# Optimization experiments

Hardware: AMD Instinct MI355X
Metric: run time of the kernel (lower is better)

The kernel has to match this reference:

```python
import jax, jax.numpy as jnp
import numpy as np

B, SEQ, DIM = 2, 2048, 1024
HEADS, DIM_HEAD = 16, 64
INNER = HEADS * DIM_HEAD
SCALE = DIM_HEAD ** -0.5


def rotate_half(x):
    # pair consecutive dims (d r) with r=2: (x1, x2) -> (-x2, x1)
    xp = x.reshape(*x.shape[:-1], -1, 2)
    x1, x2 = xp[..., 0], xp[..., 1]
    return jnp.stack((-x2, x1), axis=-1).reshape(x.shape)


def apply_rotary_emb(freqs, t):
    # freqs: [n, rot_dim] angles; t: [b, h, n, d]
    rot_dim = freqs.shape[-1]
    t_rot, t_pass = t[..., :rot_dim], t[..., rot_dim:]
    t_rot = t_rot * jnp.cos(freqs) + rotate_half(t_rot) * jnp.sin(freqs)
    return jnp.concatenate([t_rot, t_pass], axis=-1)


def setup_inputs() -> dict:
    key = jax.random.key(0)
    ks = jax.random.split(key, 4)
    x = jax.random.normal(ks[0], (B, SEQ, DIM), dtype=jnp.float32)
    mask = jnp.ones((B, SEQ), dtype=bool)
    rotary_pos_emb = jax.random.uniform(ks[1], (SEQ, DIM_HEAD), dtype=jnp.float32)
    Wqkv = jax.random.normal(ks[2], (DIM, 3 * INNER), dtype=jnp.float32) * 0.02
    Wout = jax.random.normal(ks[3], (INNER, DIM), dtype=jnp.float32) * 0.02
    bout = jnp.zeros((DIM,), dtype=jnp.float32)
    return {"x": x, "mask": mask, "rotary_pos_emb": rotary_pos_emb,
            "Wqkv": Wqkv, "Wout": Wout, "bout": bout}


def reference(x, mask, rotary_pos_emb, Wqkv, Wout, bout):
    b, n, _ = x.shape
    qkv = x @ Wqkv                                   # [b, n, 3*inner]
    q, k, v = jnp.split(qkv, 3, axis=-1)

    def to_heads(t):
        return t.reshape(b, n, HEADS, DIM_HEAD).transpose(0, 2, 1, 3)  # [b,h,n,d]

    q, k, v = to_heads(q), to_heads(k), to_heads(v)
    freqs = rotary_pos_emb[:n, :]
    # NB: original applies rotary to q, k AND v
    q = apply_rotary_emb(freqs, q)
    k = apply_rotary_emb(freqs, k)
    v = apply_rotary_emb(freqs, v)
    q = q * SCALE

    dots = jnp.einsum('bhid,bhjd->bhij', q, k)       # [b,h,n,n]
    mask_value = -jnp.finfo(dots.dtype).max
    pad = mask[:, None, None, :]                     # [b,1,1,n] keep where True
    dots = jnp.where(pad, dots, mask_value)
    idx = jnp.arange(n)
    causal = idx[None, :] > idx[:, None]             # j >= i + (j-i+1) with i==j==n
    dots = jnp.where(causal[None, None], mask_value, dots)

    attn = jax.nn.softmax(dots, axis=-1)
    out = jnp.einsum('bhij,bhjd->bhid', attn, v)     # [b,h,n,d]
    out = out.transpose(0, 2, 1, 3).reshape(b, n, INNER)
    return out @ Wout + bout
```

## Files before the change

### kernel.cpp

```cpp
#include <hip/hip_runtime.h>
#include <hip/hip_bf16.h>
#include <stdint.h>

#define DEVI __device__ __forceinline__

typedef __bf16 bf16x8 __attribute__((ext_vector_type(8)));
typedef float f32x4 __attribute__((ext_vector_type(4)));
typedef float f32x16 __attribute__((ext_vector_type(16)));

static constexpr int SEQ = 2048;
static constexpr int DIM = 1024;
static constexpr int HEADS = 16;
static constexpr int NQKV = 3072;
static constexpr int MROWS = 4096;
static constexpr float QSCALE = 0.125f;
static constexpr float LOG2E = 1.4426950408889634f;

DEVI unsigned short f2bf(float f) {
  unsigned int u = __builtin_bit_cast(unsigned int, f);
  u += 0x7FFFu + ((u >> 16) & 1u);
  return (unsigned short)(u >> 16);
}

DEVI bf16x8 ld8(const unsigned short* p) {
  return __builtin_bit_cast(bf16x8, *(const uint4*)p);
}

DEVI f32x4 mfma16(bf16x8 a, bf16x8 b, f32x4 c) {
  return __builtin_amdgcn_mfma_f32_16x16x32_bf16(a, b, c, 0, 0, 0);
}

DEVI f32x16 mfma32(bf16x8 a, bf16x8 b, f32x16 c) {
  return __builtin_amdgcn_mfma_f32_32x32x16_bf16(a, b, c, 0, 0, 0);
}

DEVI void load_lds16(const void* g, void* l) {
  __builtin_amdgcn_global_load_lds((const __attribute__((address_space(1))) void*)g,
                                   (__attribute__((address_space(3))) void*)l,
                                   16, 0, 0);
}

DEVI int swz(int row, int kelem) {
  return row * 64 + (kelem ^ ((row & 7) << 3));
}

DEVI unsigned cvtpk(float lo, float hi) {
  unsigned r;
  asm("v_cvt_pk_bf16_f32 %0, %1, %2" : "=v"(r) : "v"(lo), "v"(hi));
  return r;
}

DEVI void pl32swap(unsigned& a, unsigned& b) {
  asm volatile("v_permlane32_swap_b32 %0, %1" : "+v"(a), "+v"(b));
}
DEVI float xhalf_max(float v) { return fmaxf(v, __shfl_xor(v, 32)); }
DEVI float xhalf_sum(float v) { return v + __shfl_xor(v, 32); }

__global__ __launch_bounds__(256) void k_rope_tables(const float* __restrict__ rope,
                                                     float* __restrict__ cosb,
                                                     float* __restrict__ sinb) {
  int i = blockIdx.x * 256 + threadIdx.x;
  float f = rope[i];
  cosb[i] = cosf(f);
  sinb[i] = sinf(f);
}

__global__ __launch_bounds__(256) void k_cast_bf16(const float* __restrict__ in,
                                                   unsigned short* __restrict__ out) {
  int i = blockIdx.x * 256 + threadIdx.x;
  float4 f = *(const float4*)(in + (size_t)i * 4);
  ushort4 v;
  v.x = f2bf(f.x); v.y = f2bf(f.y); v.z = f2bf(f.z); v.w = f2bf(f.w);
  *(ushort4*)(out + (size_t)i * 4) = v;
}

__global__ __launch_bounds__(256) void k_transpose_bf16(const float* __restrict__ in,
                                                        unsigned short* __restrict__ out,
                                                        int Kd, int Nd) {
  __shared__ unsigned short T[64][68];
  const int n0 = blockIdx.x * 64, k0 = blockIdx.y * 64;
  const int rr = threadIdx.x >> 4, cc = (threadIdx.x & 15) * 4;
#pragma unroll
  for (int p = 0; p < 4; ++p) {
    const int r = p * 16 + rr;
    float4 f = *(const float4*)(in + (size_t)(k0 + r) * Nd + n0 + cc);
    T[r][cc + 0] = f2bf(f.x);
    T[r][cc + 1] = f2bf(f.y);
    T[r][cc + 2] = f2bf(f.z);
    T[r][cc + 3] = f2bf(f.w);
  }
  __syncthreads();
#pragma unroll
  for (int p = 0; p < 4; ++p) {
    const int rn = p * 16 + rr;
    ushort4 v;
    v.x = T[cc + 0][rn];
    v.y = T[cc + 1][rn];
    v.z = T[cc + 2][rn];
    v.w = T[cc + 3][rn];
    *(ushort4*)(out + (size_t)(n0 + rn) * Kd + k0 + cc) = v;
  }
}

DEVI void gemm_mainloop(const unsigned short* __restrict__ A,
                        const unsigned short* __restrict__ B, int K,
                        int m0, int n0,
                        unsigned short* As, unsigned short* Bs,
                        f32x4 (&acc)[4][4]) {
  const int lane = threadIdx.x & 63;
  const int wid = threadIdx.x >> 6;
  const int wm = wid >> 1, wn = wid & 1;
  for (int kt = 0; kt < K; kt += 32) {
    __syncthreads();
#pragma unroll
    for (int i = 0; i < 2; ++i) {
      const int chunk = wid * 2 + i;
      const int row = chunk * 16 + (lane >> 2);
      const int kc = kt + (lane & 3) * 8;
      load_lds16(A + (size_t)(m0 + row) * K + kc, As + chunk * 512);
      load_lds16(B + (size_t)(n0 + row) * K + kc, Bs + chunk * 512);
    }
    __syncthreads();
    bf16x8 af[4], bfv[4];
#pragma unroll
    for (int mi = 0; mi < 4; ++mi)
      af[mi] = ld8(&As[(wm * 64 + mi * 16 + (lane & 15)) * 32 + 8 * (lane >> 4)]);
#pragma unroll
    for (int ni = 0; ni < 4; ++ni)
      bfv[ni] = ld8(&Bs[(wn * 64 + ni * 16 + (lane & 15)) * 32 + 8 * (lane >> 4)]);
#pragma unroll
    for (int mi = 0; mi < 4; ++mi)
#pragma unroll
      for (int ni = 0; ni < 4; ++ni)
        acc[mi][ni] = mfma16(af[mi], bfv[ni], acc[mi][ni]);
  }
}

__global__ __launch_bounds__(256) void k_gemm_qkv(
    const unsigned short* __restrict__ xb, const unsigned short* __restrict__ wt,
    const float* __restrict__ cosb, const float* __restrict__ sinb,
    unsigned short* __restrict__ qb, unsigned short* __restrict__ kb,
    unsigned short* __restrict__ vb) {
  __shared__ unsigned short As[128 * 32];
  __shared__ unsigned short Bs[128 * 32];
  const int m0 = blockIdx.x * 128, n0 = blockIdx.y * 128;
  f32x4 acc[4][4] = {};
  gemm_mainloop(xb, wt, DIM, m0, n0, As, Bs, acc);
  const int lane = threadIdx.x & 63, wid = threadIdx.x >> 6;
  const int wm = wid >> 1, wn = wid & 1;
#pragma unroll
  for (int mi = 0; mi < 4; ++mi) {
#pragma unroll
    for (int ni = 0; ni < 4; ++ni) {
      const int ng = n0 + wn * 64 + ni * 16 + (lane & 15);
      const int d = ng & 63;
      const int part = ng >> 10;
      const int h = (ng & 1023) >> 6;
#pragma unroll
      for (int r = 0; r < 4; ++r) {
        const int mg = m0 + wm * 64 + mi * 16 + 4 * (lane >> 4) + r;
        const int s = mg & (SEQ - 1), b = mg >> 11;
        float v = acc[mi][ni][r];
        float p = __shfl_xor(v, 1);
        float cv = cosb[(s << 6) + d], sv = sinb[(s << 6) + d];
        float rot = v * cv + ((d & 1) ? p : -p) * sv;
        const size_t bh = (size_t)(b * HEADS + h);
        if (part == 0) {
          qb[(bh * SEQ + s) * 64 + d] = f2bf(rot * (QSCALE * LOG2E));
        } else if (part == 1) {
          kb[(bh * SEQ + s) * 64 + d] = f2bf(rot);
        } else {
          vb[(bh * 64 + d) * SEQ + s] = f2bf(rot);
        }
      }
    }
  }
}

__global__ __launch_bounds__(256) void k_flash(
    const unsigned short* __restrict__ qb, const unsigned short* __restrict__ kb,
    const unsigned short* __restrict__ vtb, unsigned short* __restrict__ ao) {
  __shared__ __align__(16) unsigned short Ks[2][2][64 * 64];
  __shared__ __align__(16) unsigned short Vt[2][2][64 * 64];
  const int bh = blockIdx.x;
  const int j = blockIdx.y;
  const int tid = threadIdx.x, lane = tid & 63, wid = tid >> 6;
  const int wq = wid >> 1, wk = wid & 1;
  const int la31 = lane & 31, h = lane >> 5;
  const unsigned short* kbh = kb + (size_t)bh * SEQ * 64;
  const unsigned short* vbh = vtb + (size_t)bh * 64 * SEQ;
  const int b = bh >> 4, hh = bh & 15;
  const int sslot = ((lane & 7) ^ (lane >> 3)) * 8;
  float* mrg = (float*)&Ks[0][0][0];
  const int mbase = wq * 2176;

  auto stage = [&](int buf, int t) {
    const int kv0 = t * 64;
#pragma unroll
    for (int i = 0; i < 4; ++i) {
      const int chunk = wq * 4 + i;
      const int row = chunk * 8 + (lane >> 3);
      load_lds16(kbh + ((size_t)(kv0 + row) << 6) + sslot, &Ks[buf][wk][chunk * 512]);
      load_lds16(vbh + (size_t)row * SEQ + kv0 + sslot, &Vt[buf][wk][chunk * 512]);
    }
  };

#pragma unroll 1
  for (int hf = 0; hf < 2; ++hf) {
    const int qt = hf == 0 ? (31 - j) : j;
    const int q0 = qt * 64 + wq * 32;
    const int qr = q0 + la31;
    const unsigned short* qp = qb + ((size_t)bh * SEQ + qr) * 64;
    bf16x8 qf0 = ld8(qp + 0 + 8 * h);
    bf16x8 qf1 = ld8(qp + 16 + 8 * h);
    bf16x8 qf2 = ld8(qp + 32 + 8 * h);
    bf16x8 qf3 = ld8(qp + 48 + 8 * h);

    f32x16 o0 = {}, o1 = {};
    float m = -1e30f, l = 0.f;
    const int nkv = qt + 1;
    const int nst = (nkv + 1) >> 1;

    if (wk < nkv) stage(0, wk);
#pragma unroll 1
    for (int st = 0; st < nst; ++st) {
      const int cur = st & 1;
      const int t = 2 * st + wk;
      __syncthreads();
      { const int tn = 2 * (st + 1) + wk; if (tn < nkv) stage(cur ^ 1, tn); }

      if (t < nkv) {
        const int kv0 = t * 64;
        const unsigned short* Kc = &Ks[cur][wk][0];
        const unsigned short* Vc = &Vt[cur][wk][0];
        f32x16 st0 = {}, st1 = {};
        __builtin_amdgcn_s_setprio(1);
#pragma unroll
        for (int ks = 0; ks < 4; ++ks) {
          bf16x8 qk = (ks == 0) ? qf0 : (ks == 1) ? qf1 : (ks == 2) ? qf2 : qf3;
          st0 = mfma32(ld8(&Kc[swz(la31, 16 * ks + 8 * h)]), qk, st0);
          st1 = mfma32(ld8(&Kc[swz(32 + la31, 16 * ks + 8 * h)]), qk, st1);
        }
        __builtin_amdgcn_s_setprio(0);
        if (kv0 + 63 > q0) {
#pragma unroll
          for (int r = 0; r < 16; ++r) {
            const int kvo = (r & 3) + 8 * (r >> 2) + 4 * h;
            st0[r] = (kv0 + kvo > qr) ? -1e30f : st0[r];
            st1[r] = (kv0 + 32 + kvo > qr) ? -1e30f : st1[r];
          }
        }
        float a8[8];
#pragma unroll
        for (int i = 0; i < 8; ++i)
          a8[i] = fmaxf(fmaxf(st0[i], st0[i + 8]), fmaxf(st1[i], st1[i + 8]));
        float a4_0 = fmaxf(a8[0], a8[4]), a4_1 = fmaxf(a8[1], a8[5]);
        float a4_2 = fmaxf(a8[2], a8[6]), a4_3 = fmaxf(a8[3], a8[7]);
        float pmax = fmaxf(fmaxf(a4_0, a4_1), fmaxf(a4_2, a4_3));
        const bool nor = __all(pmax <= m + 8.f);
        float scl = 1.f;
        if (!nor) {
          const float rowmax = xhalf_max(pmax);
          const float mnew = fmaxf(m, rowmax);
          scl = exp2f(m - mnew);
          m = mnew;
        }
#pragma unroll
        for (int r = 0; r < 16; ++r) {
          st0[r] = exp2f(st0[r] - m);
          st1[r] = exp2f(st1[r] - m);
        }
        float s8[8];
#pragma unroll
        for (int i = 0; i < 8; ++i)
          s8[i] = (st0[i] + st0[i + 8]) + (st1[i] + st1[i + 8]);
        float s4_0 = s8[0] + s8[4], s4_1 = s8[1] + s8[5];
        float s4_2 = s8[2] + s8[6], s4_3 = s8[3] + s8[7];
        float psum = (s4_0 + s4_1) + (s4_2 + s4_3);
        const float rowsum = xhalf_sum(psum);
        if (nor) {
          l += rowsum;
        } else {
          l = l * scl + rowsum;
#pragma unroll
          for (int r = 0; r < 16; ++r) { o0[r] *= scl; o1[r] *= scl; }
        }

        unsigned w0 = cvtpk(st0[0], st0[1]),   w1 = cvtpk(st0[2], st0[3]);
        unsigned w2 = cvtpk(st0[4], st0[5]),   w3 = cvtpk(st0[6], st0[7]);
        unsigned w4 = cvtpk(st0[8], st0[9]),   w5 = cvtpk(st0[10], st0[11]);
        unsigned w6 = cvtpk(st0[12], st0[13]), w7 = cvtpk(st0[14], st0[15]);
        pl32swap(w0, w2); pl32swap(w1, w3); pl32swap(w4, w6); pl32swap(w5, w7);
        const bf16x8 pa0 = __builtin_bit_cast(bf16x8, (uint4){w0, w1, w2, w3});
        const bf16x8 pa1 = __builtin_bit_cast(bf16x8, (uint4){w4, w5, w6, w7});
        unsigned x0 = cvtpk(st1[0], st1[1]),   x1 = cvtpk(st1[2], st1[3]);
        unsigned x2 = cvtpk(st1[4], st1[5]),   x3 = cvtpk(st1[6], st1[7]);
        unsigned x4 = cvtpk(st1[8], st1[9]),   x5 = cvtpk(st1[10], st1[11]);
        unsigned x6 = cvtpk(st1[12], st1[13]), x7 = cvtpk(st1[14], st1[15]);
        pl32swap(x0, x2); pl32swap(x1, x3); pl32swap(x4, x6); pl32swap(x5, x7);
        const bf16x8 pa2 = __builtin_bit_cast(bf16x8, (uint4){x0, x1, x2, x3});
        const bf16x8 pa3 = __builtin_bit_cast(bf16x8, (uint4){x4, x5, x6, x7});

        __builtin_amdgcn_s_setprio(1);
        o0 = mfma32(ld8(&Vc[swz(la31, 0 + 8 * h)]), pa0, o0);
        o0 = mfma32(ld8(&Vc[swz(la31, 16 + 8 * h)]), pa1, o0);
        o0 = mfma32(ld8(&Vc[swz(la31, 32 + 8 * h)]), pa2, o0);
        o0 = mfma32(ld8(&Vc[swz(la31, 48 + 8 * h)]), pa3, o0);
        o1 = mfma32(ld8(&Vc[swz(32 + la31, 0 + 8 * h)]), pa0, o1);
        o1 = mfma32(ld8(&Vc[swz(32 + la31, 16 + 8 * h)]), pa1, o1);
        o1 = mfma32(ld8(&Vc[swz(32 + la31, 32 + 8 * h)]), pa2, o1);
        o1 = mfma32(ld8(&Vc[swz(32 + la31, 48 + 8 * h)]), pa3, o1);
        __builtin_amdgcn_s_setprio(0);
      }
    }

    __syncthreads();
    if (wk == 1) {
#pragma unroll
      for (int s = 0; s < 8; ++s) {
        f32x4 c;
        if (s < 4) { c[0]=o0[4*s]; c[1]=o0[4*s+1]; c[2]=o0[4*s+2]; c[3]=o0[4*s+3]; }
        else       { c[0]=o1[4*(s-4)]; c[1]=o1[4*(s-4)+1]; c[2]=o1[4*(s-4)+2]; c[3]=o1[4*(s-4)+3]; }
        *(f32x4*)&mrg[mbase + lane * 32 + 4 * (s ^ (lane & 7))] = c;
      }
      mrg[mbase + 2048 + lane] = m;
      mrg[mbase + 2112 + lane] = l;
    }
    __syncthreads();
    if (wk == 0) {
      const float m1 = mrg[mbase + 2048 + lane];
      const float l1 = mrg[mbase + 2112 + lane];
      const float mM = fmaxf(m, m1);
      const float sc0 = exp2f(m - mM), sc1 = exp2f(m1 - mM);
      const float lt = l * sc0 + l1 * sc1;
      const float rl = __builtin_amdgcn_rcpf(lt);
      unsigned short* aor = ao + ((size_t)(b * SEQ + qr)) * 1024 + hh * 64;
#pragma unroll
      for (int s = 0; s < 8; ++s) {
        f32x4 c = *(const f32x4*)&mrg[mbase + lane * 32 + 4 * (s ^ (lane & 7))];
        float v0, v1, v2, v3;
        if (s < 4) {
          v0 = (o0[4*s]   * sc0 + c[0] * sc1) * rl;
          v1 = (o0[4*s+1] * sc0 + c[1] * sc1) * rl;
          v2 = (o0[4*s+2] * sc0 + c[2] * sc1) * rl;
          v3 = (o0[4*s+3] * sc0 + c[3] * sc1) * rl;
        } else {
          v0 = (o1[4*(s-4)]   * sc0 + c[0] * sc1) * rl;
          v1 = (o1[4*(s-4)+1] * sc0 + c[1] * sc1) * rl;
          v2 = (o1[4*(s-4)+2] * sc0 + c[2] * sc1) * rl;
          v3 = (o1[4*(s-4)+3] * sc0 + c[3] * sc1) * rl;
        }
        uint2 uv;
        uv.x = cvtpk(v0, v1);
        uv.y = cvtpk(v2, v3);
        *(uint2*)(aor + (s < 4 ? 8 * s : 32 + 8 * (s - 4)) + 4 * h) = uv;
      }
    }
    __syncthreads();
  }
}

__global__ __launch_bounds__(256) void k_gemm_out(
    const unsigned short* __restrict__ ao, const unsigned short* __restrict__ wt,
    const float* __restrict__ bout, float* __restrict__ out) {
  __shared__ unsigned short As[128 * 32];
  __shared__ unsigned short Bs[128 * 32];
  const int m0 = blockIdx.x * 128, n0 = blockIdx.y * 128;
  f32x4 acc[4][4] = {};
  gemm_mainloop(ao, wt, DIM, m0, n0, As, Bs, acc);
  const int lane = threadIdx.x & 63, wid = threadIdx.x >> 6;
  const int wm = wid >> 1, wn = wid & 1;
#pragma unroll
  for (int mi = 0; mi < 4; ++mi) {
#pragma unroll
    for (int ni = 0; ni < 4; ++ni) {
      const int ng = n0 + wn * 64 + ni * 16 + (lane & 15);
      const float bn = bout[ng];
#pragma unroll
      for (int r = 0; r < 4; ++r) {
        const int mg = m0 + wm * 64 + mi * 16 + 4 * (lane >> 4) + r;
        out[(size_t)mg * DIM + ng] = acc[mi][ni][r] + bn;
      }
    }
  }
}

extern "C" void kernel_launch(void* const* d_in, const int* in_sizes, int n_in,
                              void* d_out, int out_size, void* d_ws, size_t ws_size,
                              hipStream_t stream) {
  const float* x    = (const float*)d_in[0];
  const float* rope = (const float*)d_in[2];
  const float* Wqkv = (const float*)d_in[3];
  const float* Wout = (const float*)d_in[4];
  const float* bout = (const float*)d_in[5];
  float* out = (float*)d_out;

  char* ws = (char*)d_ws;
  unsigned short* xb    = (unsigned short*)(ws + 0);
  unsigned short* wqkvt = (unsigned short*)(ws + 8388608);
  unsigned short* woutt = (unsigned short*)(ws + 14680064);
  float*          cosb  = (float*)(ws + 16777216);
  float*          sinb  = (float*)(ws + 17301504);
  unsigned short* qbuf  = (unsigned short*)(ws + 17825792);
  unsigned short* kbuf  = (unsigned short*)(ws + 26214400);
  unsigned short* vbuf  = (unsigned short*)(ws + 34603008);
  unsigned short* aob   = (unsigned short*)(ws + 42991616);

  k_rope_tables<<<512, 256, 0, stream>>>(rope, cosb, sinb);
  k_cast_bf16<<<4096, 256, 0, stream>>>(x, xb);
  k_transpose_bf16<<<dim3(48, 16), 256, 0, stream>>>(Wqkv, wqkvt, DIM, NQKV);
  k_transpose_bf16<<<dim3(16, 16), 256, 0, stream>>>(Wout, woutt, DIM, DIM);
  k_gemm_qkv<<<dim3(MROWS / 128, NQKV / 128), 256, 0, stream>>>(xb, wqkvt, cosb, sinb,
                                                                qbuf, kbuf, vbuf);
  k_flash<<<dim3(32, 16), 256, 0, stream>>>(qbuf, kbuf, vbuf, aob);
  k_gemm_out<<<dim3(MROWS / 128, DIM / 128), 256, 0, stream>>>(aob, woutt, bout, out);
}
```

Measured before the change: 139.9 us.

## Fuse prep kernels, deepen GEMM K-tile to 64 with swizzle, vectorize V stores

The four preprocessing kernels (cast, rope tables, two weight transposes) are merged into one launch that dispatches on block index, removing three launch gaps. Both GEMMs now stage 64-wide K tiles in XOR-swizzled LDS, halving the number of barrier pairs per K loop and aiming to avoid bank conflicts. The transposed V write in the QKV epilogue packs four sequence positions into one 8-byte store instead of four scalar stores. LDS use per GEMM block doubles, which may reduce occupancy.

After: 132.7 us. 1.05x faster.

```diff
diff --git a/kernel.cpp b/kernel.cpp
--- a/kernel.cpp
+++ b/kernel.cpp
@@ -56,30 +56,11 @@
 DEVI float xhalf_max(float v) { return fmaxf(v, __shfl_xor(v, 32)); }
 DEVI float xhalf_sum(float v) { return v + __shfl_xor(v, 32); }
 
-__global__ __launch_bounds__(256) void k_rope_tables(const float* __restrict__ rope,
-                                                     float* __restrict__ cosb,
-                                                     float* __restrict__ sinb) {
-  int i = blockIdx.x * 256 + threadIdx.x;
-  float f = rope[i];
-  cosb[i] = cosf(f);
-  sinb[i] = sinf(f);
-}
-
-__global__ __launch_bounds__(256) void k_cast_bf16(const float* __restrict__ in,
-                                                   unsigned short* __restrict__ out) {
-  int i = blockIdx.x * 256 + threadIdx.x;
-  float4 f = *(const float4*)(in + (size_t)i * 4);
-  ushort4 v;
-  v.x = f2bf(f.x); v.y = f2bf(f.y); v.z = f2bf(f.z); v.w = f2bf(f.w);
-  *(ushort4*)(out + (size_t)i * 4) = v;
-}
-
-__global__ __launch_bounds__(256) void k_transpose_bf16(const float* __restrict__ in,
-                                                        unsigned short* __restrict__ out,
-                                                        int Kd, int Nd) {
-  __shared__ unsigned short T[64][68];
-  const int n0 = blockIdx.x * 64, k0 = blockIdx.y * 64;
-  const int rr = threadIdx.x >> 4, cc = (threadIdx.x & 15) * 4;
+DEVI void transpose_tile(const float* __restrict__ in, unsigned short* __restrict__ out,
+                         int Kd, int Nd, int bx, int by, int tid,
+                         unsigned short (*T)[68]) {
+  const int n0 = bx * 64, k0 = by * 64;
+  const int rr = tid >> 4, cc = (tid & 15) * 4;
 #pragma unroll
   for (int p = 0; p < 4; ++p) {
     const int r = p * 16 + rr;
@@ -102,37 +83,70 @@
   }
 }
 
-DEVI void gemm_mainloop(const unsigned short* __restrict__ A,
-                        const unsigned short* __restrict__ B, int K,
-                        int m0, int n0,
-                        unsigned short* As, unsigned short* Bs,
-                        f32x4 (&acc)[4][4]) {
+__global__ __launch_bounds__(256) void k_prep(
+    const float* __restrict__ x, unsigned short* __restrict__ xb,
+    const float* __restrict__ rope, float* __restrict__ cosb, float* __restrict__ sinb,
+    const float* __restrict__ Wqkv, unsigned short* __restrict__ wqkvt,
+    const float* __restrict__ Wout, unsigned short* __restrict__ woutt) {
+  __shared__ unsigned short T[64][68];
+  const int bid = blockIdx.x, tid = threadIdx.x;
+  if (bid < 4096) {
+    const int i = bid * 256 + tid;
+    float4 f = *(const float4*)(x + (size_t)i * 4);
+    ushort4 v;
+    v.x = f2bf(f.x); v.y = f2bf(f.y); v.z = f2bf(f.z); v.w = f2bf(f.w);
+    *(ushort4*)(xb + (size_t)i * 4) = v;
+  } else if (bid < 4608) {
+    const int i = (bid - 4096) * 256 + tid;
+    float f = rope[i];
+    cosb[i] = cosf(f);
+    sinb[i] = sinf(f);
+  } else if (bid < 5376) {
+    const int idx = bid - 4608;
+    transpose_tile(Wqkv, wqkvt, DIM, NQKV, idx % 48, idx / 48, tid, T);
+  } else {
+    const int idx = bid - 5376;
+    transpose_tile(Wout, woutt, DIM, DIM, idx % 16, idx / 16, tid, T);
+  }
+}
+
+DEVI void gemm_mainloop64(const unsigned short* __restrict__ A,
+                          const unsigned short* __restrict__ B, int K,
+                          int m0, int n0,
+                          unsigned short* As, unsigned short* Bs,
+                          f32x4 (&acc)[4][4]) {
   const int lane = threadIdx.x & 63;
   const int wid = threadIdx.x >> 6;
   const int wm = wid >> 1, wn = wid & 1;
-  for (int kt = 0; kt < K; kt += 32) {
+  const int rsub = lane >> 3;
+  const int ksw = ((lane & 7) ^ rsub) * 8;
+  for (int kt = 0; kt < K; kt += 64) {
     __syncthreads();
 #pragma unroll
-    for (int i = 0; i < 2; ++i) {
-      const int chunk = wid * 2 + i;
-      const int row = chunk * 16 + (lane >> 2);
-      const int kc = kt + (lane & 3) * 8;
-      load_lds16(A + (size_t)(m0 + row) * K + kc, As + chunk * 512);
-      load_lds16(B + (size_t)(n0 + row) * K + kc, Bs + chunk * 512);
+    for (int i = 0; i < 4; ++i) {
+      const int chunk = wid * 4 + i;
+      const int row = chunk * 8 + rsub;
+      load_lds16(A + (size_t)(m0 + row) * K + kt + ksw, As + chunk * 512);
+      load_lds16(B + (size_t)(n0 + row) * K + kt + ksw, Bs + chunk * 512);
     }
     __syncthreads();
-    bf16x8 af[4], bfv[4];
-#pragma unroll
-    for (int mi = 0; mi < 4; ++mi)
-      af[mi] = ld8(&As[(wm * 64 + mi * 16 + (lane & 15)) * 32 + 8 * (lane >> 4)]);
-#pragma unroll
-    for (int ni = 0; ni < 4; ++ni)
-      bfv[ni] = ld8(&Bs[(wn * 64 + ni * 16 + (lane & 15)) * 32 + 8 * (lane >> 4)]);
-#pragma unroll
-    for (int mi = 0; mi < 4; ++mi)
+#pragma unroll
+    for (int kk = 0; kk < 2; ++kk) {
+      bf16x8 af[4], bfv[4];
+#pragma unroll
+      for (int mi = 0; mi < 4; ++mi)
+        af[mi] = ld8(&As[swz(wm * 64 + mi * 16 + (lane & 15),
+                             kk * 32 + 8 * (lane >> 4))]);
 #pragma unroll
       for (int ni = 0; ni < 4; ++ni)
-        acc[mi][ni] = mfma16(af[mi], bfv[ni], acc[mi][ni]);
+        bfv[ni] = ld8(&Bs[swz(wn * 64 + ni * 16 + (lane & 15),
+                              kk * 32 + 8 * (lane >> 4))]);
+#pragma unroll
+      for (int mi = 0; mi < 4; ++mi)
+#pragma unroll
+        for (int ni = 0; ni < 4; ++ni)
+          acc[mi][ni] = mfma16(af[mi], bfv[ni], acc[mi][ni]);
+    }
   }
 }
 
@@ -141,11 +155,11 @@
     const float* __restrict__ cosb, const float* __restrict__ sinb,
     unsigned short* __restrict__ qb, unsigned short* __restrict__ kb,
     unsigned short* __restrict__ vb) {
-  __shared__ unsigned short As[128 * 32];
-  __shared__ unsigned short Bs[128 * 32];
+  __shared__ __align__(16) unsigned short As[128 * 64];
+  __shared__ __align__(16) unsigned short Bs[128 * 64];
   const int m0 = blockIdx.x * 128, n0 = blockIdx.y * 128;
   f32x4 acc[4][4] = {};
-  gemm_mainloop(xb, wt, DIM, m0, n0, As, Bs, acc);
+  gemm_mainloop64(xb, wt, DIM, m0, n0, As, Bs, acc);
   const int lane = threadIdx.x & 63, wid = threadIdx.x >> 6;
   const int wm = wid >> 1, wn = wid & 1;
 #pragma unroll
@@ -156,21 +170,34 @@
       const int d = ng & 63;
       const int part = ng >> 10;
       const int h = (ng & 1023) >> 6;
-#pragma unroll
-      for (int r = 0; r < 4; ++r) {
-        const int mg = m0 + wm * 64 + mi * 16 + 4 * (lane >> 4) + r;
-        const int s = mg & (SEQ - 1), b = mg >> 11;
-        float v = acc[mi][ni][r];
-        float p = __shfl_xor(v, 1);
-        float cv = cosb[(s << 6) + d], sv = sinb[(s << 6) + d];
-        float rot = v * cv + ((d & 1) ? p : -p) * sv;
-        const size_t bh = (size_t)(b * HEADS + h);
-        if (part == 0) {
-          qb[(bh * SEQ + s) * 64 + d] = f2bf(rot * (QSCALE * LOG2E));
-        } else if (part == 1) {
-          kb[(bh * SEQ + s) * 64 + d] = f2bf(rot);
-        } else {
-          vb[(bh * 64 + d) * SEQ + s] = f2bf(rot);
+      const int mg0 = m0 + wm * 64 + mi * 16 + 4 * (lane >> 4);
+      const int s0 = mg0 & (SEQ - 1), b = mg0 >> 11;
+      const size_t bh = (size_t)(b * HEADS + h);
+      if (part == 2) {
+        ushort4 vv;
+#pragma unroll
+        for (int r = 0; r < 4; ++r) {
+          const int s = s0 + r;
+          float v = acc[mi][ni][r];
+          float p = __shfl_xor(v, 1);
+          float cv = cosb[(s << 6) + d], sv = sinb[(s << 6) + d];
+          float rot = v * cv + ((d & 1) ? p : -p) * sv;
+          ((unsigned short*)&vv)[r] = f2bf(rot);
+        }
+        *(ushort4*)(vb + (bh * 64 + d) * SEQ + s0) = vv;
+      } else {
+#pragma unroll
+        for (int r = 0; r < 4; ++r) {
+          const int s = s0 + r;
+          float v = acc[mi][ni][r];
+          float p = __shfl_xor(v, 1);
+          float cv = cosb[(s << 6) + d], sv = sinb[(s << 6) + d];
+          float rot = v * cv + ((d & 1) ? p : -p) * sv;
+          if (part == 0) {
+            qb[(bh * SEQ + s) * 64 + d] = f2bf(rot * (QSCALE * LOG2E));
+          } else {
+            kb[(bh * SEQ + s) * 64 + d] = f2bf(rot);
+          }
         }
       }
     }
@@ -363,11 +390,11 @@
 __global__ __launch_bounds__(256) void k_gemm_out(
     const unsigned short* __restrict__ ao, const unsigned short* __restrict__ wt,
     const float* __restrict__ bout, float* __restrict__ out) {
-  __shared__ unsigned short As[128 * 32];
-  __shared__ unsigned short Bs[128 * 32];
+  __shared__ __align__(16) unsigned short As[128 * 64];
+  __shared__ __align__(16) unsigned short Bs[128 * 64];
   const int m0 = blockIdx.x * 128, n0 = blockIdx.y * 128;
   f32x4 acc[4][4] = {};
-  gemm_mainloop(ao, wt, DIM, m0, n0, As, Bs, acc);
+  gemm_mainloop64(ao, wt, DIM, m0, n0, As, Bs, acc);
   const int lane = threadIdx.x & 63, wid = threadIdx.x >> 6;
   const int wm = wid >> 1, wn = wid & 1;
 #pragma unroll
@@ -406,10 +433,7 @@
   unsigned short* vbuf  = (unsigned short*)(ws + 34603008);
   unsigned short* aob   = (unsigned short*)(ws + 42991616);
 
-  k_rope_tables<<<512, 256, 0, stream>>>(rope, cosb, sinb);
-  k_cast_bf16<<<4096, 256, 0, stream>>>(x, xb);
-  k_transpose_bf16<<<dim3(48, 16), 256, 0, stream>>>(Wqkv, wqkvt, DIM, NQKV);
-  k_transpose_bf16<<<dim3(16, 16), 256, 0, stream>>>(Wout, woutt, DIM, DIM);
+  k_prep<<<5632, 256, 0, stream>>>(x, xb, rope, cosb, sinb, Wqkv, wqkvt, Wout, woutt);
   k_gemm_qkv<<<dim3(MROWS / 128, NQKV / 128), 256, 0, stream>>>(xb, wqkvt, cosb, sinb,
                                                                 qbuf, kbuf, vbuf);
   k_flash<<<dim3(32, 16), 256, 0, stream>>>(qbuf, kbuf, vbuf, aob);
```
